# Optimization experiments

Measured on AMD Instinct MI355X. Metric: run time of the kernel, lower is better.

The kernel has to match this reference:

```python
import jax, jax.numpy as jnp
import numpy as np

B, T, C, H = 8, 2048, 1024, 64  # batch, context_length, embedding_dim, head_size


def setup_inputs() -> dict:
    key = jax.random.key(0)
    kx, kq, kk, kv = jax.random.split(key, 4)
    s = C ** -0.5  # linear-init-like scale
    return {
        "x": jax.random.normal(kx, (B, T, C), dtype=jnp.float32),
        "Wq": jax.random.normal(kq, (C, H), dtype=jnp.float32) * s,
        "Wk": jax.random.normal(kk, (C, H), dtype=jnp.float32) * s,
        "Wv": jax.random.normal(kv, (C, H), dtype=jnp.float32) * s,
    }


def reference(x, Wq, Wk, Wv):
    Bx, Tx, _ = x.shape
    q = jnp.einsum('btc,ch->bth', x, Wq)
    k = jnp.einsum('btc,ch->bth', x, Wk)
    v = jnp.einsum('btc,ch->bth', x, Wv)
    scale = k.shape[-1] ** -0.5
    scores = jnp.einsum('bth,bsh->bts', q, k) * scale  # [B, T, T]
    causal = jnp.tril(jnp.ones((Tx, Tx), dtype=bool))
    scores = jnp.where(causal, scores, -jnp.inf)
    weights = jax.nn.softmax(scores, axis=-1)
    # dropout is identity in eval mode
    out = jnp.einsum('bts,bsh->bth', weights, v)  # [B, T, H]
    return out
```

## Files before the change

### kernel.cpp

```cpp
#include <hip/hip_runtime.h>
#include <hip/hip_bf16.h>

#define BB 8
#define TT 2048
#define CC 1024
#define HH 64

typedef float f32x4 __attribute__((ext_vector_type(4)));
typedef float f32x16 __attribute__((ext_vector_type(16)));
typedef short s16x8 __attribute__((ext_vector_type(8)));

static __device__ __forceinline__ unsigned short f2bf(float f) {
    unsigned int u = __float_as_uint(f);
    u = (u + 0x7FFFu + ((u >> 16) & 1u)) >> 16;
    return (unsigned short)u;
}

static __device__ __forceinline__ unsigned cvt_pk_bf16(float lo, float hi) {
    unsigned r;
    asm("v_cvt_pk_bf16_f32 %0, %1, %2" : "=v"(r) : "v"(lo), "v"(hi));
    return r;
}

__global__ __launch_bounds__(256) void wt_kernel(
    const float* __restrict__ Wq, const float* __restrict__ Wk,
    const float* __restrict__ Wv, unsigned short* __restrict__ wTf) {
    const int e8 = blockIdx.x * 256 + threadIdx.x;
    const int lane = e8 & 63;
    const int s = (e8 >> 6) & 31;
    const int n16 = e8 >> 11;
    const int sel = n16 >> 2;
    const float* W = (sel == 0) ? Wq : ((sel == 1) ? Wk : Wv);
    const int h = ((n16 & 3) << 4) + (lane & 15);
    const int cb = s * 32 + ((lane >> 4) << 3);
    s16x8 v;
#pragma unroll
    for (int j = 0; j < 8; ++j) v[j] = (short)f2bf(W[(size_t)(cb + j) * HH + h]);
    *reinterpret_cast<s16x8*>(&wTf[(size_t)e8 * 8]) = v;
}

__global__ __launch_bounds__(512, 2) void qkv_kernel(
    const float* __restrict__ x, const unsigned short* __restrict__ wTf,
    unsigned short* __restrict__ Qf, unsigned short* __restrict__ Kf,
    unsigned short* __restrict__ Vf) {
    __shared__ unsigned short xb[2][64 * 128];
    const int tid = threadIdx.x;
    const int wv = tid >> 6, lane = tid & 63;
    const int lo = lane & 15, hi = lane >> 4;
    const int wm = wv >> 2, wn = wv & 3;
    const int rb = blockIdx.x * 64;

    const int srow = tid >> 3, sc = (tid & 7) * 16;
    const float* xsrc = &x[(size_t)(rb + srow) * CC + sc];
    const int swz = (srow & 7) << 3;
    const int wg0 = srow * 128 + (sc ^ swz);
    const int wg1 = srow * 128 + ((sc + 8) ^ swz);

    const int ar0 = (wm * 32 + lo) * 128;
    const int ar1 = ar0 + 16 * 128;
    const int aswz = (lo & 7) << 3;

    f32x4 acc[2][3];
#pragma unroll
    for (int m = 0; m < 2; ++m)
#pragma unroll
        for (int n = 0; n < 3; ++n) acc[m][n] = (f32x4){0.f, 0.f, 0.f, 0.f};

    f32x4 pf[4];
#pragma unroll
    for (int i = 0; i < 4; ++i) pf[i] = *reinterpret_cast<const f32x4*>(xsrc + 4 * i);

    s16x8 bv[3][3];
#define BLOAD(SET, SLOT)                                                       \
    {                                                                          \
        _Pragma("unroll")                                                      \
        for (int n = 0; n < 3; ++n)                                            \
            bv[SET][n] = *reinterpret_cast<const s16x8*>(                      \
                &wTf[(((size_t)(wn * 3 + n) * 32 + (SLOT)) * 64 + lane) * 8]); \
    }
    BLOAD(0, 0)
    BLOAD(1, 1)

#pragma unroll
    for (int c = 0; c < 8; ++c) {
        unsigned short* wb = xb[c & 1];
        s16x8 w0, w1;
        w0[0] = (short)f2bf(pf[0][0]); w0[1] = (short)f2bf(pf[0][1]);
        w0[2] = (short)f2bf(pf[0][2]); w0[3] = (short)f2bf(pf[0][3]);
        w0[4] = (short)f2bf(pf[1][0]); w0[5] = (short)f2bf(pf[1][1]);
        w0[6] = (short)f2bf(pf[1][2]); w0[7] = (short)f2bf(pf[1][3]);
        w1[0] = (short)f2bf(pf[2][0]); w1[1] = (short)f2bf(pf[2][1]);
        w1[2] = (short)f2bf(pf[2][2]); w1[3] = (short)f2bf(pf[2][3]);
        w1[4] = (short)f2bf(pf[3][0]); w1[5] = (short)f2bf(pf[3][1]);
        w1[6] = (short)f2bf(pf[3][2]); w1[7] = (short)f2bf(pf[3][3]);
        *reinterpret_cast<s16x8*>(&wb[wg0]) = w0;
        *reinterpret_cast<s16x8*>(&wb[wg1]) = w1;
        __syncthreads();
        if (c < 7) {
#pragma unroll
            for (int i = 0; i < 4; ++i)
                pf[i] = *reinterpret_cast<const f32x4*>(xsrc + (c + 1) * 128 + 4 * i);
        }
        const unsigned short* base = xb[c & 1];
#pragma unroll
        for (int kh = 0; kh < 4; ++kh) {
            const int slot = c * 4 + kh;
            if (slot + 2 < 32) BLOAD((slot + 2) % 3, slot + 2)
            const s16x8 a0 = *reinterpret_cast<const s16x8*>(
                &base[ar0 + ((kh * 32 + hi * 8) ^ aswz)]);
            const s16x8 a1 = *reinterpret_cast<const s16x8*>(
                &base[ar1 + ((kh * 32 + hi * 8) ^ aswz)]);
#pragma unroll
            for (int n = 0; n < 3; ++n) {
                acc[0][n] = __builtin_amdgcn_mfma_f32_16x16x32_bf16(a0, bv[slot % 3][n], acc[0][n], 0, 0, 0);
                acc[1][n] = __builtin_amdgcn_mfma_f32_16x16x32_bf16(a1, bv[slot % 3][n], acc[1][n], 0, 0, 0);
            }
        }
    }
#undef BLOAD

#pragma unroll
    for (int n = 0; n < 3; ++n) {
        const int n16 = wn * 3 + n;
        const int sel = n16 >> 2;
#pragma unroll
        for (int m = 0; m < 2; ++m) {
#pragma unroll
            for (int r = 0; r < 4; ++r) {
                const int row = rb + wm * 32 + m * 16 + 4 * hi + r;
                const int b_ = row >> 11, tok = row & (TT - 1);
                const int tile = tok >> 5;
                const unsigned short bvv = f2bf(acc[m][n][r]);
                if (sel == 0) {
                    const int s = n16, half = (lo >> 3) & 1, j = lo & 7;
                    Qf[((((size_t)b_ * 64 + tile) * 4 + s) * 64 + half * 32 + (tok & 31)) * 8 + j] = bvv;
                } else if (sel == 1) {
                    const int s = n16 - 4, half = (lo >> 3) & 1, j = lo & 7;
                    Kf[((((size_t)b_ * 64 + tile) * 4 + s) * 64 + half * 32 + (tok & 31)) * 8 + j] = bvv;
                } else {
                    const int h = (n16 - 8) * 16 + lo;
                    const int mt = h >> 5;
                    const int tt = tok & 31;
                    const int s2 = tt >> 4, hf = (tt >> 3) & 1, jj = tt & 7;
                    Vf[(((((size_t)b_ * 64 + tile) * 2 + mt) * 2 + s2) * 64 + hf * 32 + (h & 31)) * 8 + jj] = bvv;
                }
            }
        }
    }
}

__global__ __launch_bounds__(512, 4) void attn_kernel(
    const unsigned short* __restrict__ Qf, const unsigned short* __restrict__ Kf,
    const unsigned short* __restrict__ Vf, float* __restrict__ out) {
    __shared__ __align__(16) char smem[33792 + 2048];
    float (*OfL)[64][33] = reinterpret_cast<float(*)[64][33]>(smem);
    float (*Mm)[32] = reinterpret_cast<float(*)[32]>(smem + 33792);
    float (*Ml)[32] = reinterpret_cast<float(*)[32]>(smem + 33792 + 1024);

    const int tid = threadIdx.x;
    const int wv = tid >> 6, lane = tid & 63;
    const int q = lane & 31, half = lane >> 5;
    const int b = blockIdx.x & 7;
    const int qt = 63 - (blockIdx.x >> 3);
    const int qbase = qt * 32;
    const float CEXP = 0.125f * 1.44269504f;

    const unsigned short* qp = &Qf[(((size_t)b * 64 + qt) * 256 + lane) * 8];
    s16x8 qf[4];
#pragma unroll
    for (int s = 0; s < 4; ++s) qf[s] = *reinterpret_cast<const s16x8*>(qp + s * 512);

    f32x16 oA, oB;
#pragma unroll
    for (int r = 0; r < 16; ++r) { oA[r] = 0.f; oB[r] = 0.f; }
    float m = -1e30f, l = 0.f;

    for (int t = wv; t <= qt; t += 8) {
        const unsigned short* vp = &Vf[(((size_t)b * 64 + t) * 256 + lane) * 8];
        s16x8 vf[4];
#pragma unroll
        for (int i = 0; i < 4; ++i)
            vf[i] = *reinterpret_cast<const s16x8*>(vp + i * 512);
        const unsigned short* kp = &Kf[(((size_t)b * 64 + t) * 256 + lane) * 8];
        f32x16 sa;
#pragma unroll
        for (int r = 0; r < 16; ++r) sa[r] = 0.f;
#pragma unroll
        for (int s = 0; s < 4; ++s) {
            const s16x8 kf = *reinterpret_cast<const s16x8*>(kp + s * 512);
            sa = __builtin_amdgcn_mfma_f32_32x32x16_bf16(kf, qf[s], sa, 0, 0, 0);
        }
        if (t == qt) {
#pragma unroll
            for (int r = 0; r < 16; ++r) {
                const int key = 4 * half + (r & 3) + 8 * (r >> 2);
                if (key > q) sa[r] = -1e30f;
            }
        }
        float pmax = sa[0];
#pragma unroll
        for (int r = 1; r < 16; ++r) pmax = fmaxf(pmax, sa[r]);
        pmax = fmaxf(pmax, __shfl_xor(pmax, 32));
        if (!__all(pmax <= m + 64.f)) {
            const float mnew = fmaxf(m, pmax);
            const float alpha = exp2f((m - mnew) * CEXP);
            l *= alpha;
#pragma unroll
            for (int r = 0; r < 16; ++r) { oA[r] *= alpha; oB[r] *= alpha; }
            m = mnew;
        }
        float rs = 0.f;
#pragma unroll
        for (int r = 0; r < 16; ++r) {
            const float p = exp2f((sa[r] - m) * CEXP);
            sa[r] = p;
            rs += p;
        }
        l += rs + __shfl_xor(rs, 32);
        unsigned d[8];
#pragma unroll
        for (int i = 0; i < 8; ++i) d[i] = cvt_pk_bf16(sa[2 * i], sa[2 * i + 1]);
        const unsigned snd0 = half ? d[0] : d[2];
        const unsigned snd1 = half ? d[1] : d[3];
        const unsigned snd2 = half ? d[4] : d[6];
        const unsigned snd3 = half ? d[5] : d[7];
        const unsigned rcv0 = __shfl_xor(snd0, 32);
        const unsigned rcv1 = __shfl_xor(snd1, 32);
        const unsigned rcv2 = __shfl_xor(snd2, 32);
        const unsigned rcv3 = __shfl_xor(snd3, 32);
        union { unsigned u[4]; s16x8 v; } f0, f1;
        f0.u[0] = half ? rcv0 : d[0];
        f0.u[1] = half ? rcv1 : d[1];
        f0.u[2] = half ? d[2] : rcv0;
        f0.u[3] = half ? d[3] : rcv1;
        f1.u[0] = half ? rcv2 : d[4];
        f1.u[1] = half ? rcv3 : d[5];
        f1.u[2] = half ? d[6] : rcv2;
        f1.u[3] = half ? d[7] : rcv3;
        oA = __builtin_amdgcn_mfma_f32_32x32x16_bf16(vf[0], f0.v, oA, 0, 0, 0);
        oB = __builtin_amdgcn_mfma_f32_32x32x16_bf16(vf[2], f0.v, oB, 0, 0, 0);
        oA = __builtin_amdgcn_mfma_f32_32x32x16_bf16(vf[1], f1.v, oA, 0, 0, 0);
        oB = __builtin_amdgcn_mfma_f32_32x32x16_bf16(vf[3], f1.v, oB, 0, 0, 0);
    }

#define PUBLISH(slot)                                                      \
    {                                                                      \
        _Pragma("unroll")                                                  \
        for (int r = 0; r < 16; ++r) {                                     \
            const int h0 = (r & 3) + 8 * (r >> 2) + 4 * half;              \
            OfL[slot][h0][q] = oA[r];                                      \
            OfL[slot][h0 + 32][q] = oB[r];                                 \
        }                                                                  \
    }
#define MERGE(slot, srcw)                                                  \
    {                                                                      \
        const float mb = Mm[srcw][q], lb = Ml[srcw][q];                    \
        const float M = fmaxf(m, mb);                                      \
        const float wa = exp2f((m - M) * CEXP);                            \
        const float wb = exp2f((mb - M) * CEXP);                           \
        _Pragma("unroll")                                                  \
        for (int r = 0; r < 16; ++r) {                                     \
            const int h0 = (r & 3) + 8 * (r >> 2) + 4 * half;              \
            oA[r] = oA[r] * wa + OfL[slot][h0][q] * wb;                    \
            oB[r] = oB[r] * wa + OfL[slot][h0 + 32][q] * wb;               \
        }                                                                  \
        l = l * wa + lb * wb;                                              \
        m = M;                                                             \
    }

    if (lane < 32) { Mm[wv][q] = m; Ml[wv][q] = l; }
    if (wv >= 4) PUBLISH(wv - 4);
    __syncthreads();
    if (wv < 4) MERGE(wv, wv + 4);
    __syncthreads();
    if (wv == 2 || wv == 3) {
        PUBLISH(wv - 2);
        if (lane < 32) { Mm[wv][q] = m; Ml[wv][q] = l; }
    }
    __syncthreads();
    if (wv < 2) MERGE(wv, wv + 2);
    __syncthreads();
    if (wv == 1) {
        PUBLISH(1);
        if (lane < 32) { Mm[1][q] = m; Ml[1][q] = l; }
    }
    __syncthreads();
    if (wv == 0) {
        MERGE(1, 1);
        const float inv = 1.f / l;
#pragma unroll
        for (int r = 0; r < 16; ++r) {
            const int h0 = (r & 3) + 8 * (r >> 2) + 4 * half;
            OfL[0][h0][q] = oA[r] * inv;
            OfL[0][h0 + 32][q] = oB[r] * inv;
        }
    }
    __syncthreads();
#pragma unroll
    for (int i = 0; i < 4; ++i) {
        const int idx = tid + 512 * i;
        const int h = idx & 63, q2 = idx >> 6;
        out[((size_t)b * TT + qbase + q2) * HH + h] = OfL[0][h][q2];
    }
#undef PUBLISH
#undef MERGE
}

extern "C" void kernel_launch(void* const* d_in, const int* in_sizes, int n_in,
                              void* d_out, int out_size, void* d_ws, size_t ws_size,
                              hipStream_t stream) {
    (void)in_sizes; (void)n_in; (void)out_size; (void)ws_size;
    const float* x  = (const float*)d_in[0];
    const float* Wq = (const float*)d_in[1];
    const float* Wk = (const float*)d_in[2];
    const float* Wv = (const float*)d_in[3];
    float* out = (float*)d_out;

    char* ws = (char*)d_ws;
    unsigned short* wTf = (unsigned short*)ws;
    unsigned short* Qf  = (unsigned short*)(ws + 393216);
    unsigned short* Kf  = (unsigned short*)(ws + 393216 + 2097152);
    unsigned short* Vf  = (unsigned short*)(ws + 393216 + 4194304);

    wt_kernel<<<96, 256, 0, stream>>>(Wq, Wk, Wv, wTf);
    qkv_kernel<<<256, 512, 0, stream>>>(x, wTf, Qf, Kf, Vf);
    attn_kernel<<<512, 512, 0, stream>>>(Qf, Kf, Vf, out);
}
```

Before: 45.42 us.

## Halve QKV row tile, widen K chunk, stage outputs in LDS for coalesced stores

The QKV projection kernel now processes 32 rows per block instead of 64, with 256-wide K chunks over 4 iterations, and launches 512 blocks with a higher occupancy hint. Each wave does a single 16-row MFMA tile. Results are scattered into shared memory in the fragment layout and then written to Qf/Kf/Vf with 16-byte contiguous stores instead of scattered 2-byte global writes. This targets underfilled CUs and uncoalesced output stores, at the cost of reloading weight fragments for twice as many blocks and an extra LDS round trip.

```diff
diff --git a/kernel.cpp b/kernel.cpp
--- a/kernel.cpp
+++ b/kernel.cpp
@@ -39,32 +39,31 @@
     *reinterpret_cast<s16x8*>(&wTf[(size_t)e8 * 8]) = v;
 }
 
-__global__ __launch_bounds__(512, 2) void qkv_kernel(
+__global__ __launch_bounds__(512, 4) void qkv_kernel(
     const float* __restrict__ x, const unsigned short* __restrict__ wTf,
     unsigned short* __restrict__ Qf, unsigned short* __restrict__ Kf,
     unsigned short* __restrict__ Vf) {
-    __shared__ unsigned short xb[2][64 * 128];
+    __shared__ unsigned short xb[2][32 * 256];
     const int tid = threadIdx.x;
     const int wv = tid >> 6, lane = tid & 63;
     const int lo = lane & 15, hi = lane >> 4;
     const int wm = wv >> 2, wn = wv & 3;
-    const int rb = blockIdx.x * 64;
-
-    const int srow = tid >> 3, sc = (tid & 7) * 16;
+    const int rb = blockIdx.x * 32;
+    const int b_ = rb >> 11, tile = (rb & (TT - 1)) >> 5;
+
+    const int srow = tid >> 4, sc = (tid & 15) * 16;
     const float* xsrc = &x[(size_t)(rb + srow) * CC + sc];
-    const int swz = (srow & 7) << 3;
-    const int wg0 = srow * 128 + (sc ^ swz);
-    const int wg1 = srow * 128 + ((sc + 8) ^ swz);
-
-    const int ar0 = (wm * 32 + lo) * 128;
-    const int ar1 = ar0 + 16 * 128;
-    const int aswz = (lo & 7) << 3;
-
-    f32x4 acc[2][3];
-#pragma unroll
-    for (int m = 0; m < 2; ++m)
-#pragma unroll
-        for (int n = 0; n < 3; ++n) acc[m][n] = (f32x4){0.f, 0.f, 0.f, 0.f};
+    const int swz = (srow & 15) << 3;
+    const int wg0 = srow * 256 + (sc ^ swz);
+    const int wg1 = srow * 256 + ((sc + 8) ^ swz);
+
+    const int arow = wm * 16 + lo;
+    const int abase = arow * 256;
+    const int aswz = (arow & 15) << 3;
+
+    f32x4 acc[3];
+#pragma unroll
+    for (int n = 0; n < 3; ++n) acc[n] = (f32x4){0.f, 0.f, 0.f, 0.f};
 
     f32x4 pf[4];
 #pragma unroll
@@ -82,7 +81,7 @@
     BLOAD(1, 1)
 
 #pragma unroll
-    for (int c = 0; c < 8; ++c) {
+    for (int c = 0; c < 4; ++c) {
         unsigned short* wb = xb[c & 1];
         s16x8 w0, w1;
         w0[0] = (short)f2bf(pf[0][0]); w0[1] = (short)f2bf(pf[0][1]);
@@ -96,56 +95,61 @@
         *reinterpret_cast<s16x8*>(&wb[wg0]) = w0;
         *reinterpret_cast<s16x8*>(&wb[wg1]) = w1;
         __syncthreads();
-        if (c < 7) {
+        if (c < 3) {
 #pragma unroll
             for (int i = 0; i < 4; ++i)
-                pf[i] = *reinterpret_cast<const f32x4*>(xsrc + (c + 1) * 128 + 4 * i);
+                pf[i] = *reinterpret_cast<const f32x4*>(xsrc + (c + 1) * 256 + 4 * i);
         }
         const unsigned short* base = xb[c & 1];
 #pragma unroll
-        for (int kh = 0; kh < 4; ++kh) {
-            const int slot = c * 4 + kh;
+        for (int kh = 0; kh < 8; ++kh) {
+            const int slot = c * 8 + kh;
             if (slot + 2 < 32) BLOAD((slot + 2) % 3, slot + 2)
-            const s16x8 a0 = *reinterpret_cast<const s16x8*>(
-                &base[ar0 + ((kh * 32 + hi * 8) ^ aswz)]);
-            const s16x8 a1 = *reinterpret_cast<const s16x8*>(
-                &base[ar1 + ((kh * 32 + hi * 8) ^ aswz)]);
-#pragma unroll
-            for (int n = 0; n < 3; ++n) {
-                acc[0][n] = __builtin_amdgcn_mfma_f32_16x16x32_bf16(a0, bv[slot % 3][n], acc[0][n], 0, 0, 0);
-                acc[1][n] = __builtin_amdgcn_mfma_f32_16x16x32_bf16(a1, bv[slot % 3][n], acc[1][n], 0, 0, 0);
-            }
+            const s16x8 a = *reinterpret_cast<const s16x8*>(
+                &base[abase + ((kh * 32 + hi * 8) ^ aswz)]);
+#pragma unroll
+            for (int n = 0; n < 3; ++n)
+                acc[n] = __builtin_amdgcn_mfma_f32_16x16x32_bf16(a, bv[slot % 3][n], acc[n], 0, 0, 0);
         }
     }
 #undef BLOAD
 
+    __syncthreads();
+    unsigned short* fr = reinterpret_cast<unsigned short*>(xb);
 #pragma unroll
     for (int n = 0; n < 3; ++n) {
         const int n16 = wn * 3 + n;
         const int sel = n16 >> 2;
 #pragma unroll
-        for (int m = 0; m < 2; ++m) {
-#pragma unroll
-            for (int r = 0; r < 4; ++r) {
-                const int row = rb + wm * 32 + m * 16 + 4 * hi + r;
-                const int b_ = row >> 11, tok = row & (TT - 1);
-                const int tile = tok >> 5;
-                const unsigned short bvv = f2bf(acc[m][n][r]);
-                if (sel == 0) {
-                    const int s = n16, half = (lo >> 3) & 1, j = lo & 7;
-                    Qf[((((size_t)b_ * 64 + tile) * 4 + s) * 64 + half * 32 + (tok & 31)) * 8 + j] = bvv;
-                } else if (sel == 1) {
-                    const int s = n16 - 4, half = (lo >> 3) & 1, j = lo & 7;
-                    Kf[((((size_t)b_ * 64 + tile) * 4 + s) * 64 + half * 32 + (tok & 31)) * 8 + j] = bvv;
-                } else {
-                    const int h = (n16 - 8) * 16 + lo;
-                    const int mt = h >> 5;
-                    const int tt = tok & 31;
-                    const int s2 = tt >> 4, hf = (tt >> 3) & 1, jj = tt & 7;
-                    Vf[(((((size_t)b_ * 64 + tile) * 2 + mt) * 2 + s2) * 64 + hf * 32 + (h & 31)) * 8 + jj] = bvv;
-                }
+        for (int r = 0; r < 4; ++r) {
+            const int tok31 = wm * 16 + 4 * hi + r;
+            const unsigned short bvv = f2bf(acc[n][r]);
+            if (sel == 0) {
+                const int s = n16, half = (lo >> 3) & 1, j = lo & 7;
+                fr[(s * 64 + half * 32 + tok31) * 8 + j] = bvv;
+            } else if (sel == 1) {
+                const int s = n16 - 4, half = (lo >> 3) & 1, j = lo & 7;
+                fr[2048 + (s * 64 + half * 32 + tok31) * 8 + j] = bvv;
+            } else {
+                const int h = (n16 - 8) * 16 + lo;
+                const int mt = h >> 5;
+                const int s2 = tok31 >> 4, hf = (tok31 >> 3) & 1, jj = tok31 & 7;
+                fr[4096 + ((mt * 2 + s2) * 64 + hf * 32 + (h & 31)) * 8 + jj] = bvv;
             }
         }
+    }
+    __syncthreads();
+    const size_t tb = ((size_t)b_ * 64 + tile) * 2048;
+    if (tid < 256) {
+        *reinterpret_cast<s16x8*>(&Qf[tb + tid * 8]) =
+            *reinterpret_cast<const s16x8*>(&fr[tid * 8]);
+    } else {
+        *reinterpret_cast<s16x8*>(&Kf[tb + (tid - 256) * 8]) =
+            *reinterpret_cast<const s16x8*>(&fr[2048 + (tid - 256) * 8]);
+    }
+    if (tid < 256) {
+        *reinterpret_cast<s16x8*>(&Vf[tb + tid * 8]) =
+            *reinterpret_cast<const s16x8*>(&fr[4096 + tid * 8]);
     }
 }
 
@@ -323,6 +327,6 @@
     unsigned short* Vf  = (unsigned short*)(ws + 393216 + 4194304);
 
     wt_kernel<<<96, 256, 0, stream>>>(Wq, Wk, Wv, wTf);
-    qkv_kernel<<<256, 512, 0, stream>>>(x, wTf, Qf, Kf, Vf);
+    qkv_kernel<<<512, 512, 0, stream>>>(x, wTf, Qf, Kf, Vf);
     attn_kernel<<<512, 512, 0, stream>>>(Qf, Kf, Vf, out);
 }
```

Result: slower. 52.84 us (+16.3%).

## Deepen projection prefetch and stage Q/K/V epilogue through LDS for coalesced stores

Applied to the files above, without the earlier changes.

In the QKV projection kernel, the x tiles are now prefetched two chunks ahead using A/B register sets. The weight-fragment ring grows from three to four slots, so loads are issued three k-slices ahead and more global-load latency is hidden. The epilogue no longer does scattered 2-byte global writes of Q, K and V fragments. It writes them into the reused LDS buffer in the final fragment layout, then copies them out with coalesced 16-byte stores. This costs more registers (which may lower occupancy) and two extra barriers.

```diff
diff --git a/kernel.cpp b/kernel.cpp
--- a/kernel.cpp
+++ b/kernel.cpp
@@ -66,11 +66,13 @@
 #pragma unroll
         for (int n = 0; n < 3; ++n) acc[m][n] = (f32x4){0.f, 0.f, 0.f, 0.f};
 
-    f32x4 pf[4];
-#pragma unroll
-    for (int i = 0; i < 4; ++i) pf[i] = *reinterpret_cast<const f32x4*>(xsrc + 4 * i);
-
-    s16x8 bv[3][3];
+    f32x4 pfA[4], pfB[4];
+#pragma unroll
+    for (int i = 0; i < 4; ++i) pfA[i] = *reinterpret_cast<const f32x4*>(xsrc + 4 * i);
+#pragma unroll
+    for (int i = 0; i < 4; ++i) pfB[i] = *reinterpret_cast<const f32x4*>(xsrc + 128 + 4 * i);
+
+    s16x8 bv[4][3];
 #define BLOAD(SET, SLOT)                                                       \
     {                                                                          \
         _Pragma("unroll")                                                      \
@@ -80,45 +82,57 @@
     }
     BLOAD(0, 0)
     BLOAD(1, 1)
+    BLOAD(2, 2)
 
 #pragma unroll
     for (int c = 0; c < 8; ++c) {
         unsigned short* wb = xb[c & 1];
-        s16x8 w0, w1;
-        w0[0] = (short)f2bf(pf[0][0]); w0[1] = (short)f2bf(pf[0][1]);
-        w0[2] = (short)f2bf(pf[0][2]); w0[3] = (short)f2bf(pf[0][3]);
-        w0[4] = (short)f2bf(pf[1][0]); w0[5] = (short)f2bf(pf[1][1]);
-        w0[6] = (short)f2bf(pf[1][2]); w0[7] = (short)f2bf(pf[1][3]);
-        w1[0] = (short)f2bf(pf[2][0]); w1[1] = (short)f2bf(pf[2][1]);
-        w1[2] = (short)f2bf(pf[2][2]); w1[3] = (short)f2bf(pf[2][3]);
-        w1[4] = (short)f2bf(pf[3][0]); w1[5] = (short)f2bf(pf[3][1]);
-        w1[6] = (short)f2bf(pf[3][2]); w1[7] = (short)f2bf(pf[3][3]);
-        *reinterpret_cast<s16x8*>(&wb[wg0]) = w0;
-        *reinterpret_cast<s16x8*>(&wb[wg1]) = w1;
+        {
+            const f32x4* pf = (c & 1) ? pfB : pfA;
+            s16x8 w0, w1;
+            w0[0] = (short)f2bf(pf[0][0]); w0[1] = (short)f2bf(pf[0][1]);
+            w0[2] = (short)f2bf(pf[0][2]); w0[3] = (short)f2bf(pf[0][3]);
+            w0[4] = (short)f2bf(pf[1][0]); w0[5] = (short)f2bf(pf[1][1]);
+            w0[6] = (short)f2bf(pf[1][2]); w0[7] = (short)f2bf(pf[1][3]);
+            w1[0] = (short)f2bf(pf[2][0]); w1[1] = (short)f2bf(pf[2][1]);
+            w1[2] = (short)f2bf(pf[2][2]); w1[3] = (short)f2bf(pf[2][3]);
+            w1[4] = (short)f2bf(pf[3][0]); w1[5] = (short)f2bf(pf[3][1]);
+            w1[6] = (short)f2bf(pf[3][2]); w1[7] = (short)f2bf(pf[3][3]);
+            *reinterpret_cast<s16x8*>(&wb[wg0]) = w0;
+            *reinterpret_cast<s16x8*>(&wb[wg1]) = w1;
+        }
         __syncthreads();
-        if (c < 7) {
-#pragma unroll
-            for (int i = 0; i < 4; ++i)
-                pf[i] = *reinterpret_cast<const f32x4*>(xsrc + (c + 1) * 128 + 4 * i);
+        if (c < 6) {
+            if (c & 1) {
+#pragma unroll
+                for (int i = 0; i < 4; ++i)
+                    pfB[i] = *reinterpret_cast<const f32x4*>(xsrc + (c + 2) * 128 + 4 * i);
+            } else {
+#pragma unroll
+                for (int i = 0; i < 4; ++i)
+                    pfA[i] = *reinterpret_cast<const f32x4*>(xsrc + (c + 2) * 128 + 4 * i);
+            }
         }
         const unsigned short* base = xb[c & 1];
 #pragma unroll
         for (int kh = 0; kh < 4; ++kh) {
             const int slot = c * 4 + kh;
-            if (slot + 2 < 32) BLOAD((slot + 2) % 3, slot + 2)
+            if (slot + 3 < 32) BLOAD((slot + 3) & 3, slot + 3)
             const s16x8 a0 = *reinterpret_cast<const s16x8*>(
                 &base[ar0 + ((kh * 32 + hi * 8) ^ aswz)]);
             const s16x8 a1 = *reinterpret_cast<const s16x8*>(
                 &base[ar1 + ((kh * 32 + hi * 8) ^ aswz)]);
 #pragma unroll
             for (int n = 0; n < 3; ++n) {
-                acc[0][n] = __builtin_amdgcn_mfma_f32_16x16x32_bf16(a0, bv[slot % 3][n], acc[0][n], 0, 0, 0);
-                acc[1][n] = __builtin_amdgcn_mfma_f32_16x16x32_bf16(a1, bv[slot % 3][n], acc[1][n], 0, 0, 0);
+                acc[0][n] = __builtin_amdgcn_mfma_f32_16x16x32_bf16(a0, bv[slot & 3][n], acc[0][n], 0, 0, 0);
+                acc[1][n] = __builtin_amdgcn_mfma_f32_16x16x32_bf16(a1, bv[slot & 3][n], acc[1][n], 0, 0, 0);
             }
         }
     }
 #undef BLOAD
 
+    __syncthreads();
+    unsigned short* fr = reinterpret_cast<unsigned short*>(xb);
 #pragma unroll
     for (int n = 0; n < 3; ++n) {
         const int n16 = wn * 3 + n;
@@ -127,25 +141,40 @@
         for (int m = 0; m < 2; ++m) {
 #pragma unroll
             for (int r = 0; r < 4; ++r) {
-                const int row = rb + wm * 32 + m * 16 + 4 * hi + r;
-                const int b_ = row >> 11, tok = row & (TT - 1);
-                const int tile = tok >> 5;
+                const int row64 = wm * 32 + m * 16 + 4 * hi + r;
+                const int tib = row64 >> 5, tok31 = row64 & 31;
+                const int ib = tib * 6144;
                 const unsigned short bvv = f2bf(acc[m][n][r]);
                 if (sel == 0) {
                     const int s = n16, half = (lo >> 3) & 1, j = lo & 7;
-                    Qf[((((size_t)b_ * 64 + tile) * 4 + s) * 64 + half * 32 + (tok & 31)) * 8 + j] = bvv;
+                    fr[ib + (s * 64 + half * 32 + tok31) * 8 + j] = bvv;
                 } else if (sel == 1) {
                     const int s = n16 - 4, half = (lo >> 3) & 1, j = lo & 7;
-                    Kf[((((size_t)b_ * 64 + tile) * 4 + s) * 64 + half * 32 + (tok & 31)) * 8 + j] = bvv;
+                    fr[ib + 2048 + (s * 64 + half * 32 + tok31) * 8 + j] = bvv;
                 } else {
                     const int h = (n16 - 8) * 16 + lo;
                     const int mt = h >> 5;
-                    const int tt = tok & 31;
-                    const int s2 = tt >> 4, hf = (tt >> 3) & 1, jj = tt & 7;
-                    Vf[(((((size_t)b_ * 64 + tile) * 2 + mt) * 2 + s2) * 64 + hf * 32 + (h & 31)) * 8 + jj] = bvv;
+                    const int s2 = tok31 >> 4, hf = (tok31 >> 3) & 1, jj = tok31 & 7;
+                    fr[ib + 4096 + ((mt * 2 + s2) * 64 + hf * 32 + (h & 31)) * 8 + jj] = bvv;
                 }
             }
         }
+    }
+    __syncthreads();
+    const int b_ = rb >> 11;
+    const int tile0 = (rb & (TT - 1)) >> 5;
+#pragma unroll
+    for (int i = 0; i < 3; ++i) {
+        const int g = tid + 512 * i;
+        const int tib = (g >= 768) ? 1 : 0;
+        const int rem = g - tib * 768;
+        const int buf = rem >> 8;
+        const int off = rem & 255;
+        const s16x8 val = *reinterpret_cast<const s16x8*>(
+            &fr[tib * 6144 + buf * 2048 + off * 8]);
+        unsigned short* dst = (buf == 0) ? Qf : ((buf == 1) ? Kf : Vf);
+        *reinterpret_cast<s16x8*>(
+            &dst[((size_t)b_ * 64 + tile0 + tib) * 2048 + off * 8]) = val;
     }
 }
 
```

After: 42.91 us. 1.06x faster.
